# Optimization experiments

Measured on AMD Instinct MI355X. Metric: run time of the kernel, lower is better.

Reference implementation:

```python
import jax, jax.numpy as jnp
import numpy as np

B, N, M, C, NR = 8, 2048, 512, 256, 4  # batch, unknown pts, known pts, feat channels, rotation anchors
MLP = [512, 256, 256]
EPS_D, EPS_BN = 1e-8, 1e-5


def setup_inputs() -> dict:
    key = jax.random.key(0)
    ks = jax.random.split(key, 10)
    inp = {
        "unknown": jax.random.normal(ks[0], (B, N, 3), jnp.float32),
        "known": jax.random.normal(ks[1], (B, M, 3), jnp.float32),
        "unknow_feats": jax.random.normal(ks[2], (B, C, NR, N), jnp.float32),
        "known_feats": jax.random.normal(ks[3], (B, C, NR, M), jnp.float32),
    }
    # SharedMLP params: Conv2d 1x1 (no bias since bn=True) + BN gamma/beta per layer
    inp["W1"] = jax.random.normal(ks[4], (MLP[1], MLP[0]), jnp.float32) * (1.0 / np.sqrt(MLP[0]))
    inp["g1"] = jnp.ones((MLP[1],), jnp.float32)
    inp["b1"] = jnp.zeros((MLP[1],), jnp.float32)
    inp["W2"] = jax.random.normal(ks[5], (MLP[2], MLP[1]), jnp.float32) * (1.0 / np.sqrt(MLP[1]))
    inp["g2"] = jnp.ones((MLP[2],), jnp.float32)
    inp["b2"] = jnp.zeros((MLP[2],), jnp.float32)
    return inp


def _conv_bn_relu(x, W, g, b):
    # x: (B, Cin, Nr, n); 1x1 conv == channel GEMM; BN in training mode (batch stats)
    y = jnp.einsum("oi,birn->born", W, x)
    mean = jnp.mean(y, axis=(0, 2, 3), keepdims=True)
    var = jnp.var(y, axis=(0, 2, 3), keepdims=True)
    y = (y - mean) * jax.lax.rsqrt(var + EPS_BN)
    y = y * g[None, :, None, None] + b[None, :, None, None]
    return jax.nn.relu(y)


def reference(unknown, known, unknow_feats, known_feats, W1, g1, b1, W2, g2, b2):
    b_, c1, nr, n = unknow_feats.shape
    c2 = known_feats.shape[1]
    m = known_feats.shape[3]
    # --- 3-NN search: squared distances (B, n, m) ---
    d2 = (jnp.sum(unknown ** 2, -1, keepdims=True)
          + jnp.sum(known ** 2, -1)[:, None, :]
          - 2.0 * jnp.einsum("bnd,bmd->bnm", unknown, known))
    neg_top, idx = jax.lax.top_k(-d2, 3)          # (B, n, 3)
    dist2 = jnp.maximum(-neg_top, 0.0)
    # --- inverse-distance weights ---
    dist_recip = 1.0 / (jnp.sqrt(dist2) + EPS_D)
    weight = dist_recip / jnp.sum(dist_recip, axis=2, keepdims=True)  # (B, n, 3)
    # --- gather + weighted interpolation ---
    feats = known_feats.reshape(b_, c2 * nr, m).transpose(0, 2, 1)    # (B, m, C2*Nr)
    nn_features = jax.vmap(lambda f, i: f[i])(feats, idx)             # (B, n, 3, C2*Nr)
    interp = jnp.sum(weight[..., None] * nn_features, axis=2)         # (B, n, C2*Nr)
    interp = interp.transpose(0, 2, 1).reshape(b_, c2, nr, n)
    # --- concat skip + SharedMLP ---
    x = jnp.concatenate([interp, unknow_feats], axis=1)               # (B, C1+C2, Nr, n)
    x = _conv_bn_relu(x, W1, g1, b1)
    x = _conv_bn_relu(x, W2, g2, b2)
    return x
```

## Files before the change

### kernel.cpp

```cpp
#include <hip/hip_runtime.h>
#include <math.h>

#define B_   8
#define N_   2048
#define M_   512
#define C_   256
#define NR_  4
#define J_   8192
#define CIN1 512
#define BN_CNT 65536.0f
#define NSLICE 512

using f16   = _Float16;
using f16x2 = __attribute__((ext_vector_type(2))) _Float16;
using f16x8 = __attribute__((ext_vector_type(8))) _Float16;
using f32x4 = __attribute__((ext_vector_type(4))) float;

#define KNN_INSERT(e, j)                                              \
  do {                                                                \
    if ((e) < d0)      { d2v = d1; i2 = i1; d1 = d0; i1 = i0; d0 = (e); i0 = (j); } \
    else if ((e) < d1) { d2v = d1; i2 = i1; d1 = (e); i1 = (j); }     \
    else if ((e) < d2v){ d2v = (e); i2 = (j); }                       \
  } while (0)

__global__ __launch_bounds__(256) void knn_kernel(
    const float* __restrict__ unknown, const float* __restrict__ known,
    int* __restrict__ idx_out, float* __restrict__ w_out)
{
  __shared__ float4 kp[M_];
  const int b = blockIdx.y;
  const int t = threadIdx.x;
  for (int i = t; i < M_; i += 256) {
    const float kx = known[(b * M_ + i) * 3 + 0];
    const float ky = known[(b * M_ + i) * 3 + 1];
    const float kz = known[(b * M_ + i) * 3 + 2];
    kp[(i & 63) * 8 + (i >> 6)] = make_float4(kx, ky, kz, kx * kx + ky * ky + kz * kz);
  }
  __syncthreads();

  const int p = t >> 3;
  const int s = t & 7;
  const int n = blockIdx.x * 32 + p;
  const float ux = unknown[(b * N_ + n) * 3 + 0];
  const float uy = unknown[(b * N_ + n) * 3 + 1];
  const float uz = unknown[(b * N_ + n) * 3 + 2];
  const float un2 = ux * ux + uy * uy + uz * uz;

  float d0 = 3.4e38f, d1 = 3.4e38f, d2v = 3.4e38f;
  int i0 = 0, i1 = 0, i2 = 0;
#pragma unroll 8
  for (int it = 0; it < 64; ++it) {
    const float4 k4 = kp[it * 8 + s];
    const int m = s * 64 + it;
    const float d = (un2 + k4.w) - 2.0f * (ux * k4.x + uy * k4.y + uz * k4.z);
    KNN_INSERT(d, m);
  }
#pragma unroll
  for (int off = 1; off < 8; off <<= 1) {
    const float e0 = __shfl_xor(d0, off), e1 = __shfl_xor(d1, off), e2 = __shfl_xor(d2v, off);
    const int   j0 = __shfl_xor(i0, off), j1 = __shfl_xor(i1, off), j2 = __shfl_xor(i2, off);
    KNN_INSERT(e0, j0);
    KNN_INSERT(e1, j1);
    KNN_INSERT(e2, j2);
  }
  if (s == 0) {
    const float r0 = 1.0f / (sqrtf(fmaxf(d0, 0.f)) + 1e-8f);
    const float r1 = 1.0f / (sqrtf(fmaxf(d1, 0.f)) + 1e-8f);
    const float r2 = 1.0f / (sqrtf(fmaxf(d2v, 0.f)) + 1e-8f);
    const float rs = r0 + r1 + r2;
    const int base = (b * N_ + n) * 3;
    idx_out[base + 0] = i0; idx_out[base + 1] = i1; idx_out[base + 2] = i2;
    w_out[base + 0] = r0 / rs; w_out[base + 1] = r1 / rs; w_out[base + 2] = r2 / rs;
  }
}

__global__ __launch_bounds__(256) void interp_kernel(
    const float* __restrict__ kf, const int* __restrict__ idx,
    const float* __restrict__ wgt, f16* __restrict__ out)
{
  const int n0 = (blockIdx.x * 256 + threadIdx.x) * 2;
  const int c0 = blockIdx.y * 4;
  const int b = blockIdx.z >> 2, r = blockIdx.z & 3;
  const int ba = (b * N_ + n0) * 3;
  const int ia0 = idx[ba + 0], ia1 = idx[ba + 1], ia2 = idx[ba + 2];
  const int ib0 = idx[ba + 3], ib1 = idx[ba + 4], ib2 = idx[ba + 5];
  const float wa0 = wgt[ba + 0], wa1 = wgt[ba + 1], wa2 = wgt[ba + 2];
  const float wb0 = wgt[ba + 3], wb1 = wgt[ba + 4], wb2 = wgt[ba + 5];
#pragma unroll
  for (int cc = 0; cc < 4; ++cc) {
    const int c = c0 + cc;
    const float* row = kf + (((size_t)b * C_ + c) * NR_ + r) * M_;
    f16x2 v;
    v[0] = (f16)(wa0 * row[ia0] + wa1 * row[ia1] + wa2 * row[ia2]);
    v[1] = (f16)(wb0 * row[ib0] + wb1 * row[ib1] + wb2 * row[ib2]);
    *(f16x2*)&out[(((size_t)b * C_ + c) * NR_ + r) * N_ + n0] = v;
  }
}

__global__ __launch_bounds__(256) void cvt_w_kernel(
    const float* __restrict__ W1, const float* __restrict__ W2,
    f16* __restrict__ w1h, f16* __restrict__ w2h)
{
  const int i = blockIdx.x * 256 + threadIdx.x;
  if (i < 256 * 512) w1h[i] = (f16)W1[i];
  if (i < 256 * 256) w2h[i] = (f16)W2[i];
}

template <int K, bool G2>
__global__ __launch_bounds__(256, 2) void mfma_gemm(
    const f16* __restrict__ Wf,
    const f16* __restrict__ Xh, const float* __restrict__ Xf,
    const float* __restrict__ sc, const float* __restrict__ sh,
    f16* __restrict__ Yh,
    float* __restrict__ psum, float* __restrict__ psq)
{
  __shared__ __align__(16) f16 Ws[128][40];
  __shared__ __align__(16) f16 Xs[256][40];
  const int t = threadIdx.x;
  const int l = t & 63, w = t >> 6;
  const int wm = w >> 1, wn = w & 1;
  const int g = l >> 4, ln = l & 15;
  const int jb = blockIdx.x * 256;
  const int ob = blockIdx.y * 128;
  const int b  = blockIdx.z;

  f32x4 acc[4][8];
#pragma unroll
  for (int i = 0; i < 4; ++i)
#pragma unroll
    for (int j = 0; j < 8; ++j) acc[i][j] = (f32x4){0.f, 0.f, 0.f, 0.f};

  for (int kb = 0; kb < K; kb += 32) {
#pragma unroll
    for (int it = 0; it < 2; ++it) {
      const int u = it * 256 + t;
      const int o = u >> 2, kg = (u & 3) * 8;
      *(f16x8*)&Ws[o][kg] = *(const f16x8*)&Wf[(size_t)(ob + o) * K + kb + kg];
    }
#pragma unroll
    for (int it = 0; it < 2; ++it) {
      const int u = it * 256 + t;
      const int n0 = (u & 127) * 2, kg = (u >> 7) * 8;
      const int k = kb + kg;
      f16x8 v0, v1;
      if constexpr (!G2) {
        if (k < C_) {
          const f16* src = Xh + ((size_t)b * C_ + k) * J_ + jb + n0;
#pragma unroll
          for (int i = 0; i < 8; ++i) {
            const f16x2 pr = *(const f16x2*)&src[(size_t)i * J_];
            v0[i] = pr[0]; v1[i] = pr[1];
          }
        } else {
          const float* src = Xf + ((size_t)b * C_ + (k - C_)) * J_ + jb + n0;
#pragma unroll
          for (int i = 0; i < 8; ++i) {
            const float2 pr = *(const float2*)&src[(size_t)i * J_];
            v0[i] = (f16)pr.x; v1[i] = (f16)pr.y;
          }
        }
      } else {
        const f16* src = Xh + ((size_t)b * C_ + k) * J_ + jb + n0;
#pragma unroll
        for (int i = 0; i < 8; ++i) {
          const f16x2 pr = *(const f16x2*)&src[(size_t)i * J_];
          const float scv = sc[k + i], shv = sh[k + i];
          v0[i] = (f16)fmaxf((float)pr[0] * scv + shv, 0.f);
          v1[i] = (f16)fmaxf((float)pr[1] * scv + shv, 0.f);
        }
      }
      *(f16x8*)&Xs[n0][kg]     = v0;
      *(f16x8*)&Xs[n0 + 1][kg] = v1;
    }
    __syncthreads();

    f16x8 af[4], bf[8];
#pragma unroll
    for (int f = 0; f < 4; ++f)
      af[f] = *(const f16x8*)&Ws[wm * 64 + f * 16 + ln][g * 8];
#pragma unroll
    for (int f = 0; f < 8; ++f)
      bf[f] = *(const f16x8*)&Xs[wn * 128 + f * 16 + ln][g * 8];
#pragma unroll
    for (int fm = 0; fm < 4; ++fm)
#pragma unroll
      for (int fn = 0; fn < 8; ++fn)
        acc[fm][fn] = __builtin_amdgcn_mfma_f32_16x16x32_f16(af[fm], bf[fn], acc[fm][fn], 0, 0, 0);
    __syncthreads();
  }

  const int slice2 = (b * 32 + blockIdx.x) * 2 + wn;
#pragma unroll
  for (int fm = 0; fm < 4; ++fm) {
#pragma unroll
    for (int r = 0; r < 4; ++r) {
      const int o = ob + wm * 64 + fm * 16 + g * 4 + r;
      float s = 0.f, q = 0.f;
#pragma unroll
      for (int fn = 0; fn < 8; ++fn) {
        const float v = acc[fm][fn][r];
        const int j = jb + wn * 128 + fn * 16 + ln;
        Yh[((size_t)b * C_ + o) * J_ + j] = (f16)v;
        s += v; q += v * v;
      }
#pragma unroll
      for (int off = 1; off < 16; off <<= 1) {
        s += __shfl_xor(s, off);
        q += __shfl_xor(q, off);
      }
      if (ln == 0) {
        psum[(size_t)slice2 * C_ + o] = s;
        psq [(size_t)slice2 * C_ + o] = q;
      }
    }
  }
}

__global__ __launch_bounds__(256) void finalize_bn(
    const float* __restrict__ psum, const float* __restrict__ psq,
    const float* __restrict__ g, const float* __restrict__ bt,
    float* __restrict__ sc, float* __restrict__ sh)
{
  const int c = blockIdx.x, t = threadIdx.x;
  float s = 0.f, q = 0.f;
  for (int s2 = t; s2 < NSLICE; s2 += 256) {
    s += psum[(size_t)s2 * C_ + c];
    q += psq [(size_t)s2 * C_ + c];
  }
#pragma unroll
  for (int off = 1; off < 64; off <<= 1) {
    s += __shfl_xor(s, off);
    q += __shfl_xor(q, off);
  }
  __shared__ float ls[4], lq[4];
  if ((t & 63) == 0) { ls[t >> 6] = s; lq[t >> 6] = q; }
  __syncthreads();
  if (t == 0) {
    s = ls[0] + ls[1] + ls[2] + ls[3];
    q = lq[0] + lq[1] + lq[2] + lq[3];
    const float mean = s / BN_CNT;
    const float var = q / BN_CNT - mean * mean;
    const float rstd = rsqrtf(var + 1e-5f);
    const float scale = g[c] * rstd;
    sc[c] = scale;
    sh[c] = bt[c] - mean * scale;
  }
}

__global__ __launch_bounds__(256) void bn_relu_kernel(
    const f16* __restrict__ y2, float* __restrict__ out,
    const float* __restrict__ sc, const float* __restrict__ sh)
{
  const size_t i8 = (size_t)blockIdx.x * 256 + threadIdx.x;
  const int c = (int)((i8 >> 10) & (C_ - 1));
  const float s = sc[c], h = sh[c];
  const f16x8 v = *(const f16x8*)&y2[i8 * 8];
  float4 o0, o1;
  o0.x = fmaxf((float)v[0] * s + h, 0.f);
  o0.y = fmaxf((float)v[1] * s + h, 0.f);
  o0.z = fmaxf((float)v[2] * s + h, 0.f);
  o0.w = fmaxf((float)v[3] * s + h, 0.f);
  o1.x = fmaxf((float)v[4] * s + h, 0.f);
  o1.y = fmaxf((float)v[5] * s + h, 0.f);
  o1.z = fmaxf((float)v[6] * s + h, 0.f);
  o1.w = fmaxf((float)v[7] * s + h, 0.f);
  ((float4*)out)[i8 * 2]     = o0;
  ((float4*)out)[i8 * 2 + 1] = o1;
}

extern "C" void kernel_launch(void* const* d_in, const int* in_sizes, int n_in,
                              void* d_out, int out_size, void* d_ws, size_t ws_size,
                              hipStream_t stream)
{
  const float* unknown = (const float*)d_in[0];
  const float* known   = (const float*)d_in[1];
  const float* uf      = (const float*)d_in[2];
  const float* kf      = (const float*)d_in[3];
  const float* W1      = (const float*)d_in[4];
  const float* g1      = (const float*)d_in[5];
  const float* b1      = (const float*)d_in[6];
  const float* W2      = (const float*)d_in[7];
  const float* g2      = (const float*)d_in[8];
  const float* b2      = (const float*)d_in[9];
  float* out = (float*)d_out;

  float* wsf = (float*)d_ws;
  int*   idx   = (int*)d_ws;
  float* wgt   = wsf + 49152;
  float* sc1   = wsf + 98304;
  float* sh1   = wsf + 98560;
  float* sc2   = wsf + 98816;
  float* sh2   = wsf + 99072;
  float* p1s   = wsf + 99328;
  float* p1q   = wsf + 230400;
  float* p2s   = wsf + 361472;
  float* p2q   = wsf + 492544;
  f16*   w1h   = (f16*)(wsf + 623616);
  f16*   w2h   = (f16*)(wsf + 689152);
  f16*   x16   = (f16*)(wsf + 721920);
  f16*   y2h   = x16;
  f16*   y1h   = (f16*)d_out;

  cvt_w_kernel<<<512, 256, 0, stream>>>(W1, W2, w1h, w2h);
  knn_kernel<<<dim3(N_ / 32, B_), 256, 0, stream>>>(unknown, known, idx, wgt);
  interp_kernel<<<dim3(N_ / 512, C_ / 4, B_ * NR_), 256, 0, stream>>>(kf, idx, wgt, x16);

  mfma_gemm<CIN1, false><<<dim3(32, 2, 8), 256, 0, stream>>>(
      w1h, x16, uf, nullptr, nullptr, y1h, p1s, p1q);
  finalize_bn<<<256, 256, 0, stream>>>(p1s, p1q, g1, b1, sc1, sh1);

  mfma_gemm<C_, true><<<dim3(32, 2, 8), 256, 0, stream>>>(
      w2h, y1h, nullptr, sc1, sh1, y2h, p2s, p2q);
  finalize_bn<<<256, 256, 0, stream>>>(p2s, p2q, g2, b2, sc2, sh2);

  bn_relu_kernel<<<8192, 256, 0, stream>>>(y2h, out, sc2, sh2);
}
```

Measured before the change: 272.2 us.

## Prefetch GEMM tiles into registers, swizzle LDS, pre-convert skip features to fp16

The GEMM main loop now loads the next K-slice of weights and activations into registers while the current slice is being computed, which overlaps global-memory latency with MFMA work. The activation tile in LDS gets a new row mapping and an XOR column swizzle to cut bank conflicts. The skip features are converted from fp32 to fp16 in an extended prep kernel that also does the interpolation, so GEMM1 reads half-width data. In exchange this adds a full conversion pass writing into spare space in the output buffer, and the register prefetch raises register pressure.

Measured after the change: 273.4 us. Within noise of the previous version (+0.4%).

```diff
diff --git a/kernel.cpp b/kernel.cpp
--- a/kernel.cpp
+++ b/kernel.cpp
@@ -74,26 +74,43 @@
   }
 }
 
-__global__ __launch_bounds__(256) void interp_kernel(
+__global__ __launch_bounds__(256) void prep_kernel(
     const float* __restrict__ kf, const int* __restrict__ idx,
-    const float* __restrict__ wgt, f16* __restrict__ out)
-{
-  const int n0 = (blockIdx.x * 256 + threadIdx.x) * 2;
-  const int c0 = blockIdx.y * 4;
-  const int b = blockIdx.z >> 2, r = blockIdx.z & 3;
-  const int ba = (b * N_ + n0) * 3;
-  const int ia0 = idx[ba + 0], ia1 = idx[ba + 1], ia2 = idx[ba + 2];
-  const int ib0 = idx[ba + 3], ib1 = idx[ba + 4], ib2 = idx[ba + 5];
-  const float wa0 = wgt[ba + 0], wa1 = wgt[ba + 1], wa2 = wgt[ba + 2];
-  const float wb0 = wgt[ba + 3], wb1 = wgt[ba + 4], wb2 = wgt[ba + 5];
-#pragma unroll
-  for (int cc = 0; cc < 4; ++cc) {
-    const int c = c0 + cc;
-    const float* row = kf + (((size_t)b * C_ + c) * NR_ + r) * M_;
-    f16x2 v;
-    v[0] = (f16)(wa0 * row[ia0] + wa1 * row[ia1] + wa2 * row[ia2]);
-    v[1] = (f16)(wb0 * row[ib0] + wb1 * row[ib1] + wb2 * row[ib2]);
-    *(f16x2*)&out[(((size_t)b * C_ + c) * NR_ + r) * N_ + n0] = v;
+    const float* __restrict__ wgt, f16* __restrict__ x16,
+    const float* __restrict__ uf, f16* __restrict__ uf16)
+{
+  if (blockIdx.y < 64) {
+    const int n0 = (blockIdx.x * 256 + threadIdx.x) * 2;
+    const int c0 = blockIdx.y * 4;
+    const int b = blockIdx.z >> 2, r = blockIdx.z & 3;
+    const int ba = (b * N_ + n0) * 3;
+    const int ia0 = idx[ba + 0], ia1 = idx[ba + 1], ia2 = idx[ba + 2];
+    const int ib0 = idx[ba + 3], ib1 = idx[ba + 4], ib2 = idx[ba + 5];
+    const float wa0 = wgt[ba + 0], wa1 = wgt[ba + 1], wa2 = wgt[ba + 2];
+    const float wb0 = wgt[ba + 3], wb1 = wgt[ba + 4], wb2 = wgt[ba + 5];
+#pragma unroll
+    for (int cc = 0; cc < 4; ++cc) {
+      const int c = c0 + cc;
+      const float* row = kf + (((size_t)b * C_ + c) * NR_ + r) * M_;
+      f16x2 v;
+      v[0] = (f16)(wa0 * row[ia0] + wa1 * row[ia1] + wa2 * row[ia2]);
+      v[1] = (f16)(wb0 * row[ib0] + wb1 * row[ib1] + wb2 * row[ib2]);
+      *(f16x2*)&x16[(((size_t)b * C_ + c) * NR_ + r) * N_ + n0] = v;
+    }
+  } else {
+    const size_t u = ((size_t)(blockIdx.z * 32 + (blockIdx.y - 64)) * 4 + blockIdx.x) * 256 + threadIdx.x;
+    const size_t e = u * 16;
+    const float4 a0 = *(const float4*)&uf[e + 0];
+    const float4 a1 = *(const float4*)&uf[e + 4];
+    const float4 a2 = *(const float4*)&uf[e + 8];
+    const float4 a3 = *(const float4*)&uf[e + 12];
+    f16x8 v0, v1;
+    v0[0] = (f16)a0.x; v0[1] = (f16)a0.y; v0[2] = (f16)a0.z; v0[3] = (f16)a0.w;
+    v0[4] = (f16)a1.x; v0[5] = (f16)a1.y; v0[6] = (f16)a1.z; v0[7] = (f16)a1.w;
+    v1[0] = (f16)a2.x; v1[1] = (f16)a2.y; v1[2] = (f16)a2.z; v1[3] = (f16)a2.w;
+    v1[4] = (f16)a3.x; v1[5] = (f16)a3.y; v1[6] = (f16)a3.z; v1[7] = (f16)a3.w;
+    *(f16x8*)&uf16[e + 0] = v0;
+    *(f16x8*)&uf16[e + 8] = v1;
   }
 }
 
@@ -109,7 +126,7 @@
 template <int K, bool G2>
 __global__ __launch_bounds__(256, 2) void mfma_gemm(
     const f16* __restrict__ Wf,
-    const f16* __restrict__ Xh, const float* __restrict__ Xf,
+    const f16* __restrict__ Xh, const f16* __restrict__ Xh2,
     const float* __restrict__ sc, const float* __restrict__ sh,
     f16* __restrict__ Yh,
     float* __restrict__ psum, float* __restrict__ psq)
@@ -124,63 +141,77 @@
   const int ob = blockIdx.y * 128;
   const int b  = blockIdx.z;
 
+  const int wo0 = t >> 2, wkg = (t & 3) * 8;
+  const int xn0 = (t & 127) * 2;
+  const int xcc0 = t >> 7;
+  const int s0 = t & 127, s1 = 128 + (t & 127);
+  const int xswz = t & 3;
+
   f32x4 acc[4][8];
 #pragma unroll
   for (int i = 0; i < 4; ++i)
 #pragma unroll
     for (int j = 0; j < 8; ++j) acc[i][j] = (f32x4){0.f, 0.f, 0.f, 0.f};
 
-  for (int kb = 0; kb < K; kb += 32) {
+  f16x8 wr[2];
+  f16x2 xr[2][8];
+
+  auto prefetch = [&](int kb_) {
 #pragma unroll
     for (int it = 0; it < 2; ++it) {
-      const int u = it * 256 + t;
-      const int o = u >> 2, kg = (u & 3) * 8;
-      *(f16x8*)&Ws[o][kg] = *(const f16x8*)&Wf[(size_t)(ob + o) * K + kb + kg];
-    }
+      wr[it] = *(const f16x8*)&Wf[(size_t)(ob + it * 64 + wo0) * K + kb_ + wkg];
+      const int kk = kb_ + (xcc0 + it * 2) * 8;
+      const f16* src;
+      if constexpr (!G2)
+        src = (kk < C_) ? Xh + ((size_t)b * C_ + kk) * J_
+                        : Xh2 + ((size_t)b * C_ + (kk - C_)) * J_;
+      else
+        src = Xh + ((size_t)b * C_ + kk) * J_;
+      src += jb + xn0;
+#pragma unroll
+      for (int i = 0; i < 8; ++i) xr[it][i] = *(const f16x2*)&src[(size_t)i * J_];
+    }
+  };
+
+  auto store_lds = [&](int kb_) {
 #pragma unroll
     for (int it = 0; it < 2; ++it) {
-      const int u = it * 256 + t;
-      const int n0 = (u & 127) * 2, kg = (u >> 7) * 8;
-      const int k = kb + kg;
+      *(f16x8*)&Ws[it * 64 + wo0][wkg] = wr[it];
+      const int cc = xcc0 + it * 2;
+      const int col = (cc ^ xswz) * 8;
       f16x8 v0, v1;
-      if constexpr (!G2) {
-        if (k < C_) {
-          const f16* src = Xh + ((size_t)b * C_ + k) * J_ + jb + n0;
-#pragma unroll
-          for (int i = 0; i < 8; ++i) {
-            const f16x2 pr = *(const f16x2*)&src[(size_t)i * J_];
-            v0[i] = pr[0]; v1[i] = pr[1];
-          }
-        } else {
-          const float* src = Xf + ((size_t)b * C_ + (k - C_)) * J_ + jb + n0;
-#pragma unroll
-          for (int i = 0; i < 8; ++i) {
-            const float2 pr = *(const float2*)&src[(size_t)i * J_];
-            v0[i] = (f16)pr.x; v1[i] = (f16)pr.y;
-          }
+      if constexpr (G2) {
+        const int kk = kb_ + cc * 8;
+#pragma unroll
+        for (int i = 0; i < 8; ++i) {
+          const float scv = sc[kk + i], shv = sh[kk + i];
+          v0[i] = (f16)fmaxf((float)xr[it][i][0] * scv + shv, 0.f);
+          v1[i] = (f16)fmaxf((float)xr[it][i][1] * scv + shv, 0.f);
         }
       } else {
-        const f16* src = Xh + ((size_t)b * C_ + k) * J_ + jb + n0;
-#pragma unroll
-        for (int i = 0; i < 8; ++i) {
-          const f16x2 pr = *(const f16x2*)&src[(size_t)i * J_];
-          const float scv = sc[k + i], shv = sh[k + i];
-          v0[i] = (f16)fmaxf((float)pr[0] * scv + shv, 0.f);
-          v1[i] = (f16)fmaxf((float)pr[1] * scv + shv, 0.f);
-        }
+#pragma unroll
+        for (int i = 0; i < 8; ++i) { v0[i] = xr[it][i][0]; v1[i] = xr[it][i][1]; }
       }
-      *(f16x8*)&Xs[n0][kg]     = v0;
-      *(f16x8*)&Xs[n0 + 1][kg] = v1;
-    }
+      *(f16x8*)&Xs[s0][col] = v0;
+      *(f16x8*)&Xs[s1][col] = v1;
+    }
+  };
+
+  prefetch(0);
+  for (int kb = 0; kb < K; kb += 32) {
+    store_lds(kb);
     __syncthreads();
+    if (kb + 32 < K) prefetch(kb + 32);
 
     f16x8 af[4], bf[8];
 #pragma unroll
     for (int f = 0; f < 4; ++f)
       af[f] = *(const f16x8*)&Ws[wm * 64 + f * 16 + ln][g * 8];
 #pragma unroll
-    for (int f = 0; f < 8; ++f)
-      bf[f] = *(const f16x8*)&Xs[wn * 128 + f * 16 + ln][g * 8];
+    for (int f = 0; f < 8; ++f) {
+      const int sg = (ln & 1) * 128 + wn * 64 + f * 8 + (ln >> 1);
+      bf[f] = *(const f16x8*)&Xs[sg][(g ^ (sg & 3)) * 8];
+    }
 #pragma unroll
     for (int fm = 0; fm < 4; ++fm)
 #pragma unroll
@@ -300,13 +331,14 @@
   f16*   x16   = (f16*)(wsf + 721920);
   f16*   y2h   = x16;
   f16*   y1h   = (f16*)d_out;
+  f16*   uf16  = (f16*)d_out + 16777216;
 
   cvt_w_kernel<<<512, 256, 0, stream>>>(W1, W2, w1h, w2h);
   knn_kernel<<<dim3(N_ / 32, B_), 256, 0, stream>>>(unknown, known, idx, wgt);
-  interp_kernel<<<dim3(N_ / 512, C_ / 4, B_ * NR_), 256, 0, stream>>>(kf, idx, wgt, x16);
+  prep_kernel<<<dim3(4, 96, 32), 256, 0, stream>>>(kf, idx, wgt, x16, uf, uf16);
 
   mfma_gemm<CIN1, false><<<dim3(32, 2, 8), 256, 0, stream>>>(
-      w1h, x16, uf, nullptr, nullptr, y1h, p1s, p1q);
+      w1h, x16, uf16, nullptr, nullptr, y1h, p1s, p1q);
   finalize_bn<<<256, 256, 0, stream>>>(p1s, p1q, g1, b1, sc1, sh1);
 
   mfma_gemm<C_, true><<<dim3(32, 2, 8), 256, 0, stream>>>(
```
